# Optimization experiments

Measured on AMD Instinct MI355X. Metric: run time of the kernel, lower is better.

## Reference

```python
import jax, jax.numpy as jnp
import numpy as np

B, S, H, NH, HD, INTER, R = 2, 2048, 2048, 16, 128, 5504, 16


def setup_inputs() -> dict:
    key = jax.random.key(0)
    ks = iter(jax.random.split(key, 64))

    def nrm(shape, scale=0.02):
        return jax.random.normal(next(ks), shape, jnp.float32) * scale

    inp = {}
    inp["x"] = jax.random.normal(next(ks), (B, S, H), jnp.float32)
    inp["norm_weight_1"] = jnp.ones((H,), jnp.float32)
    inp["norm_weight_2"] = jnp.ones((H,), jnp.float32)
    # RoPE tables (Llama style, theta=10000)
    pos = jnp.arange(S, dtype=jnp.float32)
    inv_freq = 1.0 / (10000.0 ** (jnp.arange(0, HD, 2, dtype=jnp.float32) / HD))
    freqs = pos[:, None] * inv_freq[None, :]
    emb = jnp.concatenate([freqs, freqs], axis=-1)  # [S, HD]
    inp["cos"] = jnp.cos(emb)
    inp["sin"] = jnp.sin(emb)
    for name, (o, i) in {"q": (H, H), "k": (H, H), "v": (H, H), "o": (H, H),
                          "gate": (INTER, H), "up": (INTER, H), "down": (H, INTER)}.items():
        inp[f"w_{name}"] = nrm((o, i))
        inp[f"b_{name}"] = jnp.zeros((o,), jnp.float32)
        inp[f"w_{name}_lora_a"] = nrm((R, i))
        inp[f"w_{name}_lora_b"] = nrm((o, R))
    inp["attention_mask"] = jnp.ones((B, S), jnp.bool_)
    inp["num_heads"] = NH
    inp["head_dim"] = HD
    return inp


def _rms(x, w, eps=1e-5):
    return x * jax.lax.rsqrt(jnp.mean(x * x, axis=-1, keepdims=True) + eps) * w


def _lora(x, W, b, A, Bm):
    # base (dequantized) weight + bias + low-rank update
    return x @ W.T + b + (x @ A.T) @ Bm.T


def _rotate_half(t):
    d = t.shape[-1] // 2
    return jnp.concatenate([-t[..., d:], t[..., :d]], axis=-1)


def _rope(t, cos, sin):
    # t: [b, h, s, d]; cos/sin: [s, d]
    return t * cos + _rotate_half(t) * sin


def _forward(x, norm_weight_1, norm_weight_2, cos, sin,
             w_q, b_q, w_q_lora_a, w_q_lora_b,
             w_k, b_k, w_k_lora_a, w_k_lora_b,
             w_v, b_v, w_v_lora_a, w_v_lora_b,
             w_o, b_o, w_o_lora_a, w_o_lora_b,
             w_gate, b_gate, w_gate_lora_a, w_gate_lora_b,
             w_up, b_up, w_up_lora_a, w_up_lora_b,
             w_down, b_down, w_down_lora_a, w_down_lora_b,
             attention_mask, num_heads, head_dim):
    b, s, _ = x.shape
    xn1 = _rms(x, norm_weight_1)
    def to_heads(t):
        return t.reshape(b, s, num_heads, head_dim).transpose(0, 2, 1, 3)
    q = to_heads(_lora(xn1, w_q, b_q, w_q_lora_a, w_q_lora_b))
    k = to_heads(_lora(xn1, w_k, b_k, w_k_lora_a, w_k_lora_b))
    v = to_heads(_lora(xn1, w_v, b_v, w_v_lora_a, w_v_lora_b))
    q = _rope(q, cos, sin)
    k = _rope(k, cos, sin)
    scale = head_dim ** (-0.5)
    scores = jnp.einsum('bhqd,bhkd->bhqk', q, k) * scale
    causal = jnp.tril(jnp.ones((s, s), jnp.bool_))
    kpm = attention_mask.astype(jnp.bool_)
    mask = causal[None, None, :, :] & kpm[:, None, None, :]
    scores = jnp.where(mask, scores, jnp.float32(-1e30))
    p = jax.nn.softmax(scores, axis=-1)
    att = jnp.einsum('bhqk,bhkd->bhqd', p, v)
    att = att.transpose(0, 2, 1, 3).reshape(b, s, num_heads * head_dim)
    # pad_input re-inserts zeros at padded token positions
    att = att * kpm[:, :, None].astype(att.dtype)
    o_final = _lora(att, w_o, b_o, w_o_lora_a, w_o_lora_b)
    x_medium = x + o_final
    xn2 = _rms(x_medium, norm_weight_2)
    gate = _lora(xn2, w_gate, b_gate, w_gate_lora_a, w_gate_lora_b)
    up = _lora(xn2, w_up, b_up, w_up_lora_a, w_up_lora_b)
    hadamard = up * jax.nn.silu(gate)
    down = _lora(hadamard, w_down, b_down, w_down_lora_a, w_down_lora_b)
    return x_medium + down


def reference(x, norm_weight_1, norm_weight_2, cos, sin,
              w_q, b_q, w_q_lora_a, w_q_lora_b,
              w_k, b_k, w_k_lora_a, w_k_lora_b,
              w_v, b_v, w_v_lora_a, w_v_lora_b,
              w_o, b_o, w_o_lora_a, w_o_lora_b,
              w_gate, b_gate, w_gate_lora_a, w_gate_lora_b,
              w_up, b_up, w_up_lora_a, w_up_lora_b,
              w_down, b_down, w_down_lora_a, w_down_lora_b,
              attention_mask, num_heads, head_dim):
    return _forward(x, norm_weight_1, norm_weight_2, cos, sin,
                    w_q, b_q, w_q_lora_a, w_q_lora_b,
                    w_k, b_k, w_k_lora_a, w_k_lora_b,
                    w_v, b_v, w_v_lora_a, w_v_lora_b,
                    w_o, b_o, w_o_lora_a, w_o_lora_b,
                    w_gate, b_gate, w_gate_lora_a, w_gate_lora_b,
                    w_up, b_up, w_up_lora_a, w_up_lora_b,
                    w_down, b_down, w_down_lora_a, w_down_lora_b,
                    attention_mask, num_heads, head_dim)
```

## Files before the change

kernel.cpp:

```cpp
#include <hip/hip_runtime.h>
#include <hip/hip_bf16.h>

#define B_ 2
#define S_ 2048
#define H_ 2048
#define NH_ 16
#define HD_ 128
#define INTER_ 5504
#define M_ (B_*S_)

using bf16x8 = __attribute__((ext_vector_type(8))) short;
using f32x4  = __attribute__((ext_vector_type(4))) float;

__device__ __forceinline__ float b2f(unsigned short u) {
  union { unsigned u; float f; } c; c.u = ((unsigned)u) << 16; return c.f;
}
__device__ __forceinline__ short f2b(float f) {
  union { float f; unsigned u; } c; c.f = f;
  unsigned r = (c.u + 0x7fffu + ((c.u >> 16) & 1u)) >> 16;
  return (short)r;
}

typedef const __attribute__((address_space(1))) void* gvp;
typedef __attribute__((address_space(3))) void* lvp;
__device__ __forceinline__ void gl2lds16(const short* g, short* l) {
  __builtin_amdgcn_global_load_lds((gvp)g, (lvp)l, 16, 0, 0);
}

__global__ void k_f2b(const float* __restrict__ in, short* __restrict__ out, int n) {
  int i = (blockIdx.x * 256 + threadIdx.x) * 4;
  if (i < n) {
    float4 f = *(const float4*)(in + i);
    short4 o4; o4.x = f2b(f.x); o4.y = f2b(f.y); o4.z = f2b(f.z); o4.w = f2b(f.w);
    *(short4*)(out + i) = o4;
  }
}

__global__ __launch_bounds__(256) void k_rmsnorm(const float* __restrict__ x,
                                                 const float* __restrict__ w,
                                                 short* __restrict__ out) {
  int row = blockIdx.x;
  const float4* xr = (const float4*)(x + (long)row * H_);
  float ss = 0.f;
  float4 v[2];
#pragma unroll
  for (int it = 0; it < 2; ++it) {
    float4 t = xr[threadIdx.x + it * 256];
    v[it] = t;
    ss += t.x*t.x + t.y*t.y + t.z*t.z + t.w*t.w;
  }
#pragma unroll
  for (int o = 32; o; o >>= 1) ss += __shfl_xor(ss, o);
  __shared__ float s4[4];
  if ((threadIdx.x & 63) == 0) s4[threadIdx.x >> 6] = ss;
  __syncthreads();
  float r = rsqrtf((s4[0] + s4[1] + s4[2] + s4[3]) * (1.f / H_) + 1e-5f);
  const float4* wr = (const float4*)w;
  short4* orow = (short4*)(out + (long)row * H_);
#pragma unroll
  for (int it = 0; it < 2; ++it) {
    float4 t = v[it];
    float4 ww = wr[threadIdx.x + it * 256];
    short4 o4;
    o4.x = f2b(t.x * r * ww.x); o4.y = f2b(t.y * r * ww.y);
    o4.z = f2b(t.z * r * ww.z); o4.w = f2b(t.w * r * ww.w);
    orow[threadIdx.x + it * 256] = o4;
  }
}

__global__ __launch_bounds__(256) void k_lora_t(const short* __restrict__ Xn,
                                                const float* __restrict__ A,
                                                short* __restrict__ T2, int K) {
  int m = blockIdx.x;
  __shared__ short xrow[INTER_];
  const short* xr = Xn + (long)m * K;
  for (int i = threadIdx.x * 8; i < K; i += 256 * 8)
    *(bf16x8*)(xrow + i) = *(const bf16x8*)(xr + i);
  __syncthreads();
  int g = threadIdx.x & 15;
  int r = threadIdx.x >> 4;
  const float* ar = A + (long)r * K;
  float p = 0.f;
  int nit = K >> 6;
  for (int it = 0; it < nit; ++it) {
    int k = it * 64 + g * 4;
    float4 a = *(const float4*)(ar + k);
    short4 xv = *(const short4*)(xrow + k);
    p += b2f((unsigned short)xv.x) * a.x + b2f((unsigned short)xv.y) * a.y
       + b2f((unsigned short)xv.z) * a.z + b2f((unsigned short)xv.w) * a.w;
  }
  __shared__ float red[256];
  red[threadIdx.x] = p;
  __syncthreads();
  if (threadIdx.x < 32) {
    float s = 0.f;
    if (threadIdx.x < 16) {
      int rr = threadIdx.x;
#pragma unroll
      for (int gg = 0; gg < 16; ++gg) s += red[rr * 16 + gg];
    }
    T2[(long)m * 32 + threadIdx.x] = (threadIdx.x < 16) ? f2b(s) : (short)0;
  }
}

__global__ void k_prep_bm2(const float* __restrict__ Bm, short* __restrict__ Bm2, int N) {
  int i = blockIdx.x * 256 + threadIdx.x;
  if (i >= N * 32) return;
  int c = i & 31, n = i >> 5;
  Bm2[i] = (c < 16) ? f2b(Bm[(long)n * 16 + c]) : (short)0;
}

__global__ __launch_bounds__(256) void k_gemm_qkv(
    const short* __restrict__ A, const short* __restrict__ W,
    const float* __restrict__ bias,
    const short* __restrict__ T2, const short* __restrict__ Bm2,
    const float* __restrict__ cs, const float* __restrict__ sn,
    short* __restrict__ out, int do_rope) {
  const int K = H_;
  __shared__ short As[128 * 32];
  __shared__ short Bs[128 * 32];
  int t = threadIdx.x;
  int lane = t & 63, wave = t >> 6;
  int row0 = blockIdx.y * 128;
  int col0 = blockIdx.x * 128;
  int lr = lane & 15, lk = (lane >> 4) << 3;
  int srow = t >> 2, skc = t & 3;
  const short* Ag0 = A + (long)(row0 + srow) * K + skc * 8;
  const short* Ag1 = A + (long)(row0 + 64 + srow) * K + skc * 8;
  const short* Wg0 = W + (long)(col0 + srow) * K + skc * 8;
  const short* Wg1 = W + (long)(col0 + 64 + srow) * K + skc * 8;
  short* Al0 = As + wave * 512;
  short* Al1 = As + 2048 + wave * 512;
  short* Bl0 = Bs + wave * 512;
  short* Bl1 = Bs + 2048 + wave * 512;
  f32x4 acc[2][8] = {};
  for (int k0 = 0; k0 < K; k0 += 32) {
    gl2lds16(Ag0 + k0, Al0);
    gl2lds16(Ag1 + k0, Al1);
    gl2lds16(Wg0 + k0, Bl0);
    gl2lds16(Wg1 + k0, Bl1);
    __syncthreads();
    bf16x8 a[2], b[8];
#pragma unroll
    for (int i = 0; i < 2; ++i) a[i] = *(const bf16x8*)(As + (wave * 32 + i * 16 + lr) * 32 + lk);
#pragma unroll
    for (int j = 0; j < 8; ++j) b[j] = *(const bf16x8*)(Bs + (j * 16 + lr) * 32 + lk);
#pragma unroll
    for (int i = 0; i < 2; ++i)
#pragma unroll
      for (int j = 0; j < 8; ++j)
        acc[i][j] = __builtin_amdgcn_mfma_f32_16x16x32_bf16(a[i], b[j], acc[i][j], 0, 0, 0);
    __syncthreads();
  }
  {
    bf16x8 a[2], b[8];
#pragma unroll
    for (int i = 0; i < 2; ++i) a[i] = *(const bf16x8*)(T2 + (long)(row0 + wave * 32 + i * 16 + lr) * 32 + lk);
#pragma unroll
    for (int j = 0; j < 8; ++j) b[j] = *(const bf16x8*)(Bm2 + (long)(col0 + j * 16 + lr) * 32 + lk);
#pragma unroll
    for (int i = 0; i < 2; ++i)
#pragma unroll
      for (int j = 0; j < 8; ++j)
        acc[i][j] = __builtin_amdgcn_mfma_f32_16x16x32_bf16(a[i], b[j], acc[i][j], 0, 0, 0);
  }
  int rquad = (lane >> 4) * 4;
  int head = blockIdx.x;
#pragma unroll
  for (int i = 0; i < 2; ++i) {
#pragma unroll
    for (int tt = 0; tt < 4; ++tt) {
      int row = row0 + wave * 32 + i * 16 + rquad + tt;
      int bb = row >> 11, sr = row & (S_ - 1);
      float vals[8];
#pragma unroll
      for (int j = 0; j < 8; ++j) vals[j] = acc[i][j][tt] + bias[col0 + j * 16 + lr];
      long obase = ((long)(bb * NH_ + head) * S_ + sr) * HD_;
      if (do_rope) {
#pragma unroll
        for (int j = 0; j < 8; ++j) {
          int d = j * 16 + lr;
          float rot = (j < 4) ? -vals[j + 4] : vals[j - 4];
          out[obase + d] = f2b(vals[j] * cs[sr * HD_ + d] + rot * sn[sr * HD_ + d]);
        }
      } else {
#pragma unroll
        for (int j = 0; j < 8; ++j) out[obase + j * 16 + lr] = f2b(vals[j]);
      }
    }
  }
}

__global__ __launch_bounds__(256) void k_gemm(
    const short* __restrict__ A, const short* __restrict__ W,
    const float* __restrict__ bias,
    const short* __restrict__ T2, const short* __restrict__ Bm2,
    const float* __restrict__ resid, const short* gatebf, int do_silu,
    float* __restrict__ outf, short* outb,
    int N, int K) {
  __shared__ short As[128 * 32];
  __shared__ short Bs[128 * 32];
  int t = threadIdx.x;
  int lane = t & 63, wave = t >> 6;
  int wm = wave >> 1, wn = wave & 1;
  int row0 = blockIdx.y * 128;
  int col0 = blockIdx.x * 128;
  int lr = lane & 15, lk = (lane >> 4) << 3;
  int srow = t >> 2, skc = t & 3;
  const short* Ag0 = A + (long)(row0 + srow) * K + skc * 8;
  const short* Ag1 = A + (long)(row0 + 64 + srow) * K + skc * 8;
  const short* Wg0 = W + (long)(col0 + srow) * K + skc * 8;
  const short* Wg1 = W + (long)(col0 + 64 + srow) * K + skc * 8;
  short* Al0 = As + wave * 512;
  short* Al1 = As + 2048 + wave * 512;
  short* Bl0 = Bs + wave * 512;
  short* Bl1 = Bs + 2048 + wave * 512;
  f32x4 acc[4][4] = {};
  for (int k0 = 0; k0 < K; k0 += 32) {
    gl2lds16(Ag0 + k0, Al0);
    gl2lds16(Ag1 + k0, Al1);
    gl2lds16(Wg0 + k0, Bl0);
    gl2lds16(Wg1 + k0, Bl1);
    __syncthreads();
    bf16x8 a[4], b[4];
#pragma unroll
    for (int i = 0; i < 4; ++i) a[i] = *(const bf16x8*)(As + (wm * 64 + i * 16 + lr) * 32 + lk);
#pragma unroll
    for (int j = 0; j < 4; ++j) b[j] = *(const bf16x8*)(Bs + (wn * 64 + j * 16 + lr) * 32 + lk);
#pragma unroll
    for (int i = 0; i < 4; ++i)
#pragma unroll
      for (int j = 0; j < 4; ++j)
        acc[i][j] = __builtin_amdgcn_mfma_f32_16x16x32_bf16(a[i], b[j], acc[i][j], 0, 0, 0);
    __syncthreads();
  }
  {
    bf16x8 a[4], b[4];
#pragma unroll
    for (int i = 0; i < 4; ++i) a[i] = *(const bf16x8*)(T2 + (long)(row0 + wm * 64 + i * 16 + lr) * 32 + lk);
#pragma unroll
    for (int j = 0; j < 4; ++j) b[j] = *(const bf16x8*)(Bm2 + (long)(col0 + wn * 64 + j * 16 + lr) * 32 + lk);
#pragma unroll
    for (int i = 0; i < 4; ++i)
#pragma unroll
      for (int j = 0; j < 4; ++j)
        acc[i][j] = __builtin_amdgcn_mfma_f32_16x16x32_bf16(a[i], b[j], acc[i][j], 0, 0, 0);
  }
  int rquad = (lane >> 4) * 4;
#pragma unroll
  for (int i = 0; i < 4; ++i) {
#pragma unroll
    for (int j = 0; j < 4; ++j) {
      int col = col0 + wn * 64 + j * 16 + lr;
      float bc = bias[col];
#pragma unroll
      for (int tt = 0; tt < 4; ++tt) {
        int row = row0 + wm * 64 + i * 16 + rquad + tt;
        long idx = (long)row * N + col;
        float v2 = acc[i][j][tt] + bc;
        if (do_silu) v2 = v2 / (1.f + __expf(-v2));
        if (gatebf) v2 *= b2f((unsigned short)gatebf[idx]);
        if (resid) v2 += resid[idx];
        if (outf) outf[idx] = v2;
        else outb[idx] = f2b(v2);
      }
    }
  }
}

__global__ __launch_bounds__(256) void k_vtrans(const short* __restrict__ in,
                                                short* __restrict__ out) {
  __shared__ short tb[64][72];
  int t = threadIdx.x;
  int s0 = blockIdx.x * 64, d0 = blockIdx.y * 64, bh = blockIdx.z;
  long ibase = (long)bh * S_ * HD_;
  long obase = (long)bh * HD_ * S_;
  int r = t >> 2, c = t & 3;
#pragma unroll
  for (int cc = 0; cc < 2; ++cc) {
    int ch = c + cc * 4;
    *(uint4*)&tb[r][ch * 8] = *(const uint4*)(in + ibase + (long)(s0 + r) * HD_ + d0 + ch * 8);
  }
  __syncthreads();
  int d = t >> 2;
#pragma unroll
  for (int cc = 0; cc < 2; ++cc) {
    int ch = c + cc * 4;
    short v[8];
#pragma unroll
    for (int ii = 0; ii < 8; ++ii) v[ii] = tb[ch * 8 + ii][d];
    *(uint4*)(out + obase + (long)(d0 + d) * S_ + s0 + ch * 8) = *(uint4*)v;
  }
}

__global__ __launch_bounds__(256) void k_attn(const short* __restrict__ Q,
                                              const short* __restrict__ Kg,
                                              const short* __restrict__ Vt,
                                              short* __restrict__ att) {
  __shared__ __align__(16) short Kls[2][4][64 * 32];
  __shared__ __align__(16) short Vls[2][2][128 * 32];
  __shared__ __align__(16) short Pl[4][32 * 72];
  __shared__ float al[4][32];
  __shared__ float ll[4][32];
  int t = threadIdx.x, lane = t & 63, wave = t >> 6;
  int lr = lane & 15, quad = lane >> 4;
  int bh = blockIdx.x & 31;
  int qb = 15 - (blockIdx.x >> 5);
  int q0 = qb * 128;
  int qlo = q0 + wave * 32;
  long base = (long)bh * S_ * HD_;
  long vbase = (long)bh * HD_ * S_;
  const float c1 = 0.08838834764831845f * 1.44269504089f;
  bf16x8 qf[2][4];
#pragma unroll
  for (int i = 0; i < 2; ++i)
#pragma unroll
    for (int ks = 0; ks < 4; ++ks)
      qf[i][ks] = *(const bf16x8*)(Q + base + (long)(qlo + i * 16 + lr) * HD_ + ks * 32 + quad * 8);
  f32x4 oacc[8][2] = {};
  float m_i[2][4], l_i[2][4];
#pragma unroll
  for (int i = 0; i < 2; ++i)
#pragma unroll
    for (int tt = 0; tt < 4; ++tt) { m_i[i][tt] = -3.0e38f; l_i[i][tt] = 0.f; }
  int sk_row = lane >> 2, sk_c = lane & 3;
  auto stage = [&](int buf, int kb) {
    int kk0 = kb << 6;
#pragma unroll
    for (int i = 0; i < 4; ++i)
      gl2lds16(Kg + base + (long)(kk0 + i * 16 + sk_row) * HD_ + wave * 32 + sk_c * 8,
               &Kls[buf][wave][i * 512]);
#pragma unroll
    for (int kv = 0; kv < 2; ++kv)
#pragma unroll
      for (int db = 0; db < 2; ++db)
        gl2lds16(Vt + vbase + (long)(wave * 32 + db * 16 + sk_row) * S_ + kk0 + kv * 32 + sk_c * 8,
                 &Vls[buf][kv][(wave * 32 + db * 16) * 32]);
  };
  int kbmax = (q0 + 127) >> 6;
  stage(0, 0);
  int cur = 0;
  for (int kb = 0; kb <= kbmax; ++kb) {
    int kk0 = kb << 6;
    asm volatile("s_waitcnt vmcnt(0) lgkmcnt(0)" ::: "memory");
    __syncthreads();
    if (kb < kbmax) stage(cur ^ 1, kb + 1);
    if (kk0 <= qlo + 31) {
      f32x4 s[2][4] = {};
#pragma unroll
      for (int ks = 0; ks < 4; ++ks) {
        bf16x8 kf[4];
#pragma unroll
        for (int j = 0; j < 4; ++j) kf[j] = *(const bf16x8*)&Kls[cur][ks][(j * 16 + lr) * 32 + quad * 8];
#pragma unroll
        for (int i = 0; i < 2; ++i)
#pragma unroll
          for (int j = 0; j < 4; ++j)
            s[i][j] = __builtin_amdgcn_mfma_f32_16x16x32_bf16(qf[i][ks], kf[j], s[i][j], 0, 0, 0);
      }
      if (kk0 + 63 > qlo) {
#pragma unroll
        for (int i = 0; i < 2; ++i)
#pragma unroll
          for (int j = 0; j < 4; ++j) {
            int key = kk0 + j * 16 + lr;
#pragma unroll
            for (int tt = 0; tt < 4; ++tt) {
              int qrow = qlo + i * 16 + quad * 4 + tt;
              if (key > qrow) s[i][j][tt] = -1.0e30f;
            }
          }
      }
#pragma unroll
      for (int i = 0; i < 2; ++i) {
#pragma unroll
        for (int tt = 0; tt < 4; ++tt) {
          float mx = fmaxf(fmaxf(s[i][0][tt], s[i][1][tt]), fmaxf(s[i][2][tt], s[i][3][tt]));
#pragma unroll
          for (int o = 1; o < 16; o <<= 1) mx = fmaxf(mx, __shfl_xor(mx, o));
          float mold = m_i[i][tt];
          float mnew = fmaxf(mold, mx);
          float alpha = exp2f((mold - mnew) * c1);
          float mc = mnew * c1;
          float rs = 0.f;
#pragma unroll
          for (int j = 0; j < 4; ++j) {
            float p = exp2f(s[i][j][tt] * c1 - mc);
            s[i][j][tt] = p;
            rs += p;
          }
#pragma unroll
          for (int o = 1; o < 16; o <<= 1) rs += __shfl_xor(rs, o);
          l_i[i][tt] = l_i[i][tt] * alpha + rs;
          m_i[i][tt] = mnew;
          if (lr == 0) al[wave][i * 16 + quad * 4 + tt] = alpha;
        }
      }
#pragma unroll
      for (int i = 0; i < 2; ++i)
#pragma unroll
        for (int j = 0; j < 4; ++j)
#pragma unroll
          for (int tt = 0; tt < 4; ++tt)
            Pl[wave][(i * 16 + quad * 4 + tt) * 72 + j * 16 + lr] = f2b(s[i][j][tt]);
#pragma unroll
      for (int i2 = 0; i2 < 2; ++i2) {
        float aq = al[wave][i2 * 16 + lr];
#pragma unroll
        for (int mi = 0; mi < 8; ++mi) {
          oacc[mi][i2][0] *= aq; oacc[mi][i2][1] *= aq;
          oacc[mi][i2][2] *= aq; oacc[mi][i2][3] *= aq;
        }
      }
#pragma unroll
      for (int kv = 0; kv < 2; ++kv) {
        bf16x8 pf[2];
#pragma unroll
        for (int i2 = 0; i2 < 2; ++i2)
          pf[i2] = *(const bf16x8*)&Pl[wave][(i2 * 16 + lr) * 72 + kv * 32 + quad * 8];
#pragma unroll
        for (int mi = 0; mi < 8; ++mi) {
          bf16x8 vfr = *(const bf16x8*)&Vls[cur][kv][(mi * 16 + lr) * 32 + quad * 8];
#pragma unroll
          for (int i2 = 0; i2 < 2; ++i2)
            oacc[mi][i2] = __builtin_amdgcn_mfma_f32_16x16x32_bf16(vfr, pf[i2], oacc[mi][i2], 0, 0, 0);
        }
      }
    }
    cur ^= 1;
  }
#pragma unroll
  for (int i = 0; i < 2; ++i)
#pragma unroll
    for (int tt = 0; tt < 4; ++tt)
      if (lr == 0) ll[wave][i * 16 + quad * 4 + tt] = l_i[i][tt];
  int b = bh >> 4, h = bh & (NH_ - 1);
#pragma unroll
  for (int i2 = 0; i2 < 2; ++i2) {
    float inv = 1.f / ll[wave][i2 * 16 + lr];
    int q_abs = qlo + i2 * 16 + lr;
    long ob = ((long)(b * S_ + q_abs)) * H_ + h * HD_;
#pragma unroll
    for (int mi = 0; mi < 8; ++mi) {
      short4 o4;
      o4.x = f2b(oacc[mi][i2][0] * inv);
      o4.y = f2b(oacc[mi][i2][1] * inv);
      o4.z = f2b(oacc[mi][i2][2] * inv);
      o4.w = f2b(oacc[mi][i2][3] * inv);
      *(short4*)(att + ob + mi * 16 + quad * 4) = o4;
    }
  }
}

extern "C" void kernel_launch(void* const* d_in, const int* in_sizes, int n_in,
                              void* d_out, int out_size, void* d_ws, size_t ws_size,
                              hipStream_t stream) {
  const float* x    = (const float*)d_in[0];
  const float* nw1  = (const float*)d_in[1];
  const float* nw2  = (const float*)d_in[2];
  const float* cosb = (const float*)d_in[3];
  const float* sinb = (const float*)d_in[4];
  const float *W[7], *Bias[7], *La[7], *Lb[7];
  for (int p = 0; p < 7; ++p) {
    W[p]    = (const float*)d_in[5 + p * 4];
    Bias[p] = (const float*)d_in[6 + p * 4];
    La[p]   = (const float*)d_in[7 + p * 4];
    Lb[p]   = (const float*)d_in[8 + p * 4];
  }
  const int wsz[7] = {H_*H_, H_*H_, H_*H_, H_*H_, INTER_*H_, INTER_*H_, INTER_*H_};

  char* ws = (char*)d_ws;
  size_t off = 0;
  short* wbuf = (short*)(ws + off); off += (size_t)INTER_ * H_ * 2;
  short* T2   = (short*)(ws + off); off += (size_t)M_ * 32 * 2;
  short* Bm2  = (short*)(ws + off); off += (size_t)INTER_ * 32 * 2;
  short* xn   = (short*)(ws + off); off += (size_t)M_ * H_ * 2;
  char*  regC = ws + off;           off += (size_t)M_ * H_ * 2 * 3;
  short* gact = (short*)(ws + off); off += (size_t)M_ * INTER_ * 2;
  short* qr = (short*)regC;
  short* kr = (short*)(regC + (size_t)M_ * H_ * 2);
  short* vr = (short*)(regC + (size_t)M_ * H_ * 2 * 2);
  float* xmed = (float*)regC;
  short* vt   = gact;
  short* attb = xn;
  float* outp = (float*)d_out;

  auto conv = [&](int p) {
    k_f2b<<<dim3((wsz[p] / 4 + 255) / 256), dim3(256), 0, stream>>>(W[p], wbuf, wsz[p]);
  };
  auto lora = [&](int p, const short* Ain, int K, int N) {
    k_lora_t<<<dim3(M_), dim3(256), 0, stream>>>(Ain, La[p], T2, K);
    k_prep_bm2<<<dim3((N * 32 + 255) / 256), dim3(256), 0, stream>>>(Lb[p], Bm2, N);
  };

  k_rmsnorm<<<dim3(M_), dim3(256), 0, stream>>>(x, nw1, xn);
  conv(0); lora(0, xn, H_, H_);
  k_gemm_qkv<<<dim3(NH_, M_ / 128), dim3(256), 0, stream>>>(xn, wbuf, Bias[0], T2, Bm2, cosb, sinb, qr, 1);
  conv(1); lora(1, xn, H_, H_);
  k_gemm_qkv<<<dim3(NH_, M_ / 128), dim3(256), 0, stream>>>(xn, wbuf, Bias[1], T2, Bm2, cosb, sinb, kr, 1);
  conv(2); lora(2, xn, H_, H_);
  k_gemm_qkv<<<dim3(NH_, M_ / 128), dim3(256), 0, stream>>>(xn, wbuf, Bias[2], T2, Bm2, cosb, sinb, vr, 0);
  k_vtrans<<<dim3(S_ / 64, HD_ / 64, B_ * NH_), dim3(256), 0, stream>>>(vr, vt);
  k_attn<<<dim3(B_ * NH_ * (S_ / 128)), dim3(256), 0, stream>>>(qr, kr, vt, attb);
  conv(3); lora(3, attb, H_, H_);
  k_gemm<<<dim3(H_ / 128, M_ / 128), dim3(256), 0, stream>>>(
      attb, wbuf, Bias[3], T2, Bm2, x, nullptr, 0, xmed, nullptr, H_, H_);
  k_rmsnorm<<<dim3(M_), dim3(256), 0, stream>>>(xmed, nw2, xn);
  conv(4); lora(4, xn, H_, INTER_);
  k_gemm<<<dim3(INTER_ / 128, M_ / 128), dim3(256), 0, stream>>>(
      xn, wbuf, Bias[4], T2, Bm2, nullptr, nullptr, 1, nullptr, gact, INTER_, H_);
  conv(5); lora(5, xn, H_, INTER_);
  k_gemm<<<dim3(INTER_ / 128, M_ / 128), dim3(256), 0, stream>>>(
      xn, wbuf, Bias[5], T2, Bm2, nullptr, gact, 0, nullptr, gact, INTER_, H_);
  conv(6); lora(6, gact, INTER_, H_);
  k_gemm<<<dim3(H_ / 128, M_ / 128), dim3(256), 0, stream>>>(
      gact, wbuf, Bias[6], T2, Bm2, xmed, nullptr, 0, outp, nullptr, H_, INTER_);
}
```

Before: 1.374 ms.

## Double-buffer LDS tiles in QKV and generic GEMM kernels

```diff
diff --git a/kernel.cpp b/kernel.cpp
--- a/kernel.cpp
+++ b/kernel.cpp
@@ -117,8 +117,8 @@
     const float* __restrict__ cs, const float* __restrict__ sn,
     short* __restrict__ out, int do_rope) {
   const int K = H_;
-  __shared__ short As[128 * 32];
-  __shared__ short Bs[128 * 32];
+  __shared__ short As[2][128 * 32];
+  __shared__ short Bs[2][128 * 32];
   int t = threadIdx.x;
   int lane = t & 63, wave = t >> 6;
   int row0 = blockIdx.y * 128;
@@ -129,28 +129,30 @@
   const short* Ag1 = A + (long)(row0 + 64 + srow) * K + skc * 8;
   const short* Wg0 = W + (long)(col0 + srow) * K + skc * 8;
   const short* Wg1 = W + (long)(col0 + 64 + srow) * K + skc * 8;
-  short* Al0 = As + wave * 512;
-  short* Al1 = As + 2048 + wave * 512;
-  short* Bl0 = Bs + wave * 512;
-  short* Bl1 = Bs + 2048 + wave * 512;
+  auto stage = [&](int buf, int k0) {
+    gl2lds16(Ag0 + k0, &As[buf][wave * 512]);
+    gl2lds16(Ag1 + k0, &As[buf][2048 + wave * 512]);
+    gl2lds16(Wg0 + k0, &Bs[buf][wave * 512]);
+    gl2lds16(Wg1 + k0, &Bs[buf][2048 + wave * 512]);
+  };
   f32x4 acc[2][8] = {};
+  stage(0, 0);
+  int cur = 0;
   for (int k0 = 0; k0 < K; k0 += 32) {
-    gl2lds16(Ag0 + k0, Al0);
-    gl2lds16(Ag1 + k0, Al1);
-    gl2lds16(Wg0 + k0, Bl0);
-    gl2lds16(Wg1 + k0, Bl1);
+    asm volatile("s_waitcnt vmcnt(0) lgkmcnt(0)" ::: "memory");
     __syncthreads();
+    if (k0 + 32 < K) stage(cur ^ 1, k0 + 32);
     bf16x8 a[2], b[8];
 #pragma unroll
-    for (int i = 0; i < 2; ++i) a[i] = *(const bf16x8*)(As + (wave * 32 + i * 16 + lr) * 32 + lk);
-#pragma unroll
-    for (int j = 0; j < 8; ++j) b[j] = *(const bf16x8*)(Bs + (j * 16 + lr) * 32 + lk);
+    for (int i = 0; i < 2; ++i) a[i] = *(const bf16x8*)(&As[cur][(wave * 32 + i * 16 + lr) * 32 + lk]);
+#pragma unroll
+    for (int j = 0; j < 8; ++j) b[j] = *(const bf16x8*)(&Bs[cur][(j * 16 + lr) * 32 + lk]);
 #pragma unroll
     for (int i = 0; i < 2; ++i)
 #pragma unroll
       for (int j = 0; j < 8; ++j)
         acc[i][j] = __builtin_amdgcn_mfma_f32_16x16x32_bf16(a[i], b[j], acc[i][j], 0, 0, 0);
-    __syncthreads();
+    cur ^= 1;
   }
   {
     bf16x8 a[2], b[8];
@@ -198,8 +200,8 @@
     const float* __restrict__ resid, const short* gatebf, int do_silu,
     float* __restrict__ outf, short* outb,
     int N, int K) {
-  __shared__ short As[128 * 32];
-  __shared__ short Bs[128 * 32];
+  __shared__ short As[2][128 * 32];
+  __shared__ short Bs[2][128 * 32];
   int t = threadIdx.x;
   int lane = t & 63, wave = t >> 6;
   int wm = wave >> 1, wn = wave & 1;
@@ -211,28 +213,30 @@
   const short* Ag1 = A + (long)(row0 + 64 + srow) * K + skc * 8;
   const short* Wg0 = W + (long)(col0 + srow) * K + skc * 8;
   const short* Wg1 = W + (long)(col0 + 64 + srow) * K + skc * 8;
-  short* Al0 = As + wave * 512;
-  short* Al1 = As + 2048 + wave * 512;
-  short* Bl0 = Bs + wave * 512;
-  short* Bl1 = Bs + 2048 + wave * 512;
+  auto stage = [&](int buf, int k0) {
+    gl2lds16(Ag0 + k0, &As[buf][wave * 512]);
+    gl2lds16(Ag1 + k0, &As[buf][2048 + wave * 512]);
+    gl2lds16(Wg0 + k0, &Bs[buf][wave * 512]);
+    gl2lds16(Wg1 + k0, &Bs[buf][2048 + wave * 512]);
+  };
   f32x4 acc[4][4] = {};
+  stage(0, 0);
+  int cur = 0;
   for (int k0 = 0; k0 < K; k0 += 32) {
-    gl2lds16(Ag0 + k0, Al0);
-    gl2lds16(Ag1 + k0, Al1);
-    gl2lds16(Wg0 + k0, Bl0);
-    gl2lds16(Wg1 + k0, Bl1);
+    asm volatile("s_waitcnt vmcnt(0) lgkmcnt(0)" ::: "memory");
     __syncthreads();
+    if (k0 + 32 < K) stage(cur ^ 1, k0 + 32);
     bf16x8 a[4], b[4];
 #pragma unroll
-    for (int i = 0; i < 4; ++i) a[i] = *(const bf16x8*)(As + (wm * 64 + i * 16 + lr) * 32 + lk);
-#pragma unroll
-    for (int j = 0; j < 4; ++j) b[j] = *(const bf16x8*)(Bs + (wn * 64 + j * 16 + lr) * 32 + lk);
+    for (int i = 0; i < 4; ++i) a[i] = *(const bf16x8*)(&As[cur][(wm * 64 + i * 16 + lr) * 32 + lk]);
+#pragma unroll
+    for (int j = 0; j < 4; ++j) b[j] = *(const bf16x8*)(&Bs[cur][(wn * 64 + j * 16 + lr) * 32 + lk]);
 #pragma unroll
     for (int i = 0; i < 4; ++i)
 #pragma unroll
       for (int j = 0; j < 4; ++j)
         acc[i][j] = __builtin_amdgcn_mfma_f32_16x16x32_bf16(a[i], b[j], acc[i][j], 0, 0, 0);
-    __syncthreads();
+    cur ^= 1;
   }
   {
     bf16x8 a[4], b[4];
```

Measured after the change: 1.351 ms. About the same (-1.7%).
